# Kernel tuning notes

Measured on AMD Instinct MI355X. Metric: run time of the kernel, lower is better.

The kernel has to match this reference:

```python
import jax, jax.numpy as jnp
import numpy as np
import math

B, L, D, H = 8, 1000, 1024, 16
HD = D // H

def setup_inputs() -> dict:
    key = jax.random.key(0)
    k1, k2, k3 = jax.random.split(key, 3)
    s_in = 1.0 / math.sqrt(D)
    x = jax.random.normal(k1, (B, L, D), dtype=jnp.float32)
    Wqkv = jax.random.normal(k2, (D, 3 * D), dtype=jnp.float32) * s_in
    bqkv = jnp.zeros((3 * D,), dtype=jnp.float32)
    Wo = jax.random.normal(k3, (D, D), dtype=jnp.float32) * s_in
    bo = jnp.zeros((D,), dtype=jnp.float32)
    return {"x": x, "Wqkv": Wqkv, "bqkv": bqkv, "Wo": Wo, "bo": bo}

def reference(x, Wqkv, bqkv, Wo, bo):
    b, l, d = x.shape
    qkv = x @ Wqkv + bqkv                      # [B,L,3D]
    q, k, v = jnp.split(qkv, 3, axis=-1)       # each [B,L,D]
    q = q.reshape(b, l, H, HD)
    k = k.reshape(b, l, H, HD)
    v = v.reshape(b, l, H, HD)
    scale = 1.0 / math.sqrt(HD)
    att = jnp.einsum('blhd,bmhd->bhlm', q, k) * scale   # [B,H,L,L]
    causal = jnp.tril(jnp.ones((l, l), dtype=bool))      # [L,L]
    att = jnp.where(causal[None, None, :, :], att, -jnp.inf)
    att = jax.nn.softmax(att, axis=-1)
    out = jnp.einsum('bhlm,bmhd->blhd', att, v).reshape(b, l, d)
    return out @ Wo + bo
```

## Files before the change

### kernel.cpp

```cpp
#include <hip/hip_runtime.h>
#include <hip/hip_bf16.h>

typedef unsigned short u16;
typedef unsigned int u32;
typedef __attribute__((ext_vector_type(8))) __bf16 bf16x8;
typedef __attribute__((ext_vector_type(4))) float f32x4;
typedef __attribute__((ext_vector_type(4))) u32 u32x4;
typedef __attribute__((ext_vector_type(4))) u16 u16x4;

#define LQ 1000
#define MM 8000

__device__ __forceinline__ u16 f2bf(float f){
  __bf16 h = (__bf16)f;
  return __builtin_bit_cast(u16, h);
}
__device__ __forceinline__ void async_copy16(const void* g, void* l){
  __builtin_amdgcn_global_load_lds((const __attribute__((address_space(1))) u32*)g,
                                   (__attribute__((address_space(3))) u32*)l, 16, 0, 0);
}

__global__ __launch_bounds__(256)
void kcvt(const float* __restrict__ src, u16* __restrict__ dst, long n){
  const long i = ((long)blockIdx.x * 256 + threadIdx.x) * 4;
  if (i + 3 >= n) {
    for (long j = i; j < n; j++) dst[j] = f2bf(src[j]);
    return;
  }
  const float4 v = *(const float4*)&src[i];
  u16x4 o; o.x = f2bf(v.x); o.y = f2bf(v.y); o.z = f2bf(v.z); o.w = f2bf(v.w);
  *(u16x4*)&dst[i] = o;
}

__global__ __launch_bounds__(256)
void ktranspose_cvt(const float* __restrict__ src, u16* __restrict__ dst, int R, int C){
  __shared__ u16 tile[32][33];
  const int tx = threadIdx.x & 31, ty = threadIdx.x >> 5;
  const long bx = (long)blockIdx.x * 32, by = (long)blockIdx.y * 32;
  #pragma unroll
  for (int i = 0; i < 32; i += 8) tile[ty + i][tx] = f2bf(src[(by + ty + i) * C + bx + tx]);
  __syncthreads();
  #pragma unroll
  for (int i = 0; i < 32; i += 8) dst[(bx + ty + i) * R + by + tx] = tile[tx][ty + i];
}

template<int EPI>
__global__ __launch_bounds__(256)
void gemm128(const u16* __restrict__ A, const u16* __restrict__ BT, const float* __restrict__ bias,
             u16* __restrict__ O0, u16* __restrict__ O1, u16* __restrict__ O2,
             float* __restrict__ OF)
{
  constexpr int K = 1024;
  __shared__ __align__(16) u16 As[2][128 * 32];
  __shared__ __align__(16) u16 Bs[2][128 * 32];
  const int t = threadIdx.x, lane = t & 63, wave = t >> 6;
  const int quad = lane >> 4, l15 = lane & 15;
  const int m0 = blockIdx.y * 128, n0 = blockIdx.x * 128;
  const int wm = (wave >> 1) * 64, wn = (wave & 1) * 64;

  f32x4 acc[4][4] = {};

  const int srow = t >> 2, scol = (t & 3) * 8;
  const long aoff0 = (long)min(m0 + srow,      MM - 1) * K + scol;
  const long aoff1 = (long)min(m0 + srow + 64, MM - 1) * K + scol;
  const long boff0 = (long)(n0 + srow)      * K + scol;
  const long boff1 = (long)(n0 + srow + 64) * K + scol;
  char* AsB0 = (char*)As[0] + wave * 1024;
  char* AsB1 = (char*)As[1] + wave * 1024;
  char* BsB0 = (char*)Bs[0] + wave * 1024;
  char* BsB1 = (char*)Bs[1] + wave * 1024;

  for (int kt = 0; kt < K; kt += 64) {
    __syncthreads();
    async_copy16(A  + aoff0 + kt,      AsB0);
    async_copy16(A  + aoff1 + kt,      AsB0 + 4096);
    async_copy16(BT + boff0 + kt,      BsB0);
    async_copy16(BT + boff1 + kt,      BsB0 + 4096);
    async_copy16(A  + aoff0 + kt + 32, AsB1);
    async_copy16(A  + aoff1 + kt + 32, AsB1 + 4096);
    async_copy16(BT + boff0 + kt + 32, BsB1);
    async_copy16(BT + boff1 + kt + 32, BsB1 + 4096);
    __syncthreads();
    #pragma unroll
    for (int half = 0; half < 2; half++) {
      bf16x8 af[4], bfv[4];
      #pragma unroll
      for (int i = 0; i < 4; i++) af[i]  = *(const bf16x8*)&As[half][(wm + i * 16 + l15) * 32 + quad * 8];
      #pragma unroll
      for (int i = 0; i < 4; i++) bfv[i] = *(const bf16x8*)&Bs[half][(wn + i * 16 + l15) * 32 + quad * 8];
      #pragma unroll
      for (int mi = 0; mi < 4; mi++)
        #pragma unroll
        for (int ni = 0; ni < 4; ni++)
          acc[mi][ni] = __builtin_amdgcn_mfma_f32_16x16x32_bf16(af[mi], bfv[ni], acc[mi][ni], 0, 0, 0);
    }
  }

  float bs[4]; int cols[4];
  #pragma unroll
  for (int ni = 0; ni < 4; ni++) { cols[ni] = n0 + wn + ni * 16 + l15; bs[ni] = bias[cols[ni]]; }

  #pragma unroll
  for (int mi = 0; mi < 4; mi++) {
    #pragma unroll
    for (int r = 0; r < 4; r++) {
      const int row = m0 + wm + mi * 16 + quad * 4 + r;
      if (row >= MM) continue;
      if (EPI == 0) {
        const int b = row / 1000, l = row - b * 1000;
        #pragma unroll
        for (int ni = 0; ni < 4; ni++) {
          const u16 o = f2bf(acc[mi][ni][r] + bs[ni]);
          const int col = cols[ni];
          const int which = col >> 10, hh = (col >> 6) & 15, dd = col & 63;
          const int bh = b * 16 + hh;
          if      (which == 0) O0[((long)bh * LQ + l) * 64 + dd] = o;
          else if (which == 1) O1[((long)bh * LQ + l) * 64 + dd] = o;
          else                 O2[((long)bh * 64 + dd) * LQ + l] = o;
        }
      } else {
        #pragma unroll
        for (int ni = 0; ni < 4; ni++)
          OF[(long)row * 1024 + cols[ni]] = acc[mi][ni][r] + bs[ni];
      }
    }
  }
}

__global__ __launch_bounds__(256)
void attn_kernel(const u16* __restrict__ Qb, const u16* __restrict__ Kb,
                 const u16* __restrict__ VTb, u16* __restrict__ AO)
{
  __shared__ __align__(16) u16 Ps[4][2][16 * 40];
  const int t = threadIdx.x, lane = t & 63, wave = t >> 6;
  const int quad = lane >> 4, l15 = lane & 15;
  const int bh = blockIdx.y;
  const int c = blockIdx.x * 4 + wave;
  const u16* Q  = Qb  + (long)bh * LQ * 64;
  const u16* Kp = Kb  + (long)bh * LQ * 64;
  const u16* VT = VTb + (long)bh * 64 * LQ;
  const int b = bh >> 4, h = bh & 15;
  const float sscale = 0.18033688011112042f;

  for (int pass = 0; pass < 2; ++pass) {
    const int chunk = pass ? (31 - c) : c;
    const int qbase = chunk * 32;
    const int nkt = chunk + 1;

    int qv[2]; bf16x8 bq0[2], bq1[2];
    #pragma unroll
    for (int g = 0; g < 2; g++) {
      qv[g] = qbase + g * 16 + l15;
      const int qc = min(qv[g], LQ - 1);
      bq0[g] = *(const bf16x8*)&Q[(long)qc * 64 +      quad * 8];
      bq1[g] = *(const bf16x8*)&Q[(long)qc * 64 + 32 + quad * 8];
    }

    float l_p[2] = { 0.f, 0.f };
    f32x4 o[2][4] = {};

    bf16x8 pa00, pa01, pa10, pa11, pav0, pav1, pav2, pav3;
    {
      const int krA = min(l15, LQ - 1), krB = min(16 + l15, LQ - 1);
      pa00 = *(const bf16x8*)&Kp[(long)krA * 64 +      quad * 8];
      pa01 = *(const bf16x8*)&Kp[(long)krA * 64 + 32 + quad * 8];
      pa10 = *(const bf16x8*)&Kp[(long)krB * 64 +      quad * 8];
      pa11 = *(const bf16x8*)&Kp[(long)krB * 64 + 32 + quad * 8];
      const int vcol = min(quad * 8, LQ - 8);
      pav0 = *(const bf16x8*)&VT[(long)( 0 + l15) * LQ + vcol];
      pav1 = *(const bf16x8*)&VT[(long)(16 + l15) * LQ + vcol];
      pav2 = *(const bf16x8*)&VT[(long)(32 + l15) * LQ + vcol];
      pav3 = *(const bf16x8*)&VT[(long)(48 + l15) * LQ + vcol];
    }

    for (int kk = 0; kk < nkt; ++kk) {
      const int k0 = kk * 32;
      const bool lastt = (kk + 1 == nkt);
      const bf16x8 a00 = pa00, a01 = pa01, a10 = pa10, a11 = pa11;
      bf16x8 av[4] = { pav0, pav1, pav2, pav3 };
      if (!lastt) {
        const int n0k = k0 + 32;
        const int krA = min(n0k + l15, LQ - 1), krB = min(n0k + 16 + l15, LQ - 1);
        pa00 = *(const bf16x8*)&Kp[(long)krA * 64 +      quad * 8];
        pa01 = *(const bf16x8*)&Kp[(long)krA * 64 + 32 + quad * 8];
        pa10 = *(const bf16x8*)&Kp[(long)krB * 64 +      quad * 8];
        pa11 = *(const bf16x8*)&Kp[(long)krB * 64 + 32 + quad * 8];
        const int vcol = min(n0k + quad * 8, LQ - 8);
        pav0 = *(const bf16x8*)&VT[(long)( 0 + l15) * LQ + vcol];
        pav1 = *(const bf16x8*)&VT[(long)(16 + l15) * LQ + vcol];
        pav2 = *(const bf16x8*)&VT[(long)(32 + l15) * LQ + vcol];
        pav3 = *(const bf16x8*)&VT[(long)(48 + l15) * LQ + vcol];
      }

      #pragma unroll
      for (int g = 0; g < 2; g++) {
        const f32x4 z = {};
        f32x4 s0 = __builtin_amdgcn_mfma_f32_16x16x32_bf16(a00, bq0[g], z, 0, 0, 0);
        s0       = __builtin_amdgcn_mfma_f32_16x16x32_bf16(a01, bq1[g], s0, 0, 0, 0);
        f32x4 s1 = __builtin_amdgcn_mfma_f32_16x16x32_bf16(a10, bq0[g], z, 0, 0, 0);
        s1       = __builtin_amdgcn_mfma_f32_16x16x32_bf16(a11, bq1[g], s1, 0, 0, 0);

        float p0[4], p1[4];
        if (lastt) {
          const int q = qv[g];
          #pragma unroll
          for (int r = 0; r < 4; r++) {
            const int key0 = k0 + quad * 4 + r;
            p0[r] = __builtin_amdgcn_exp2f((key0      <= q) ? s0[r] * sscale : -3.0e38f);
            p1[r] = __builtin_amdgcn_exp2f((key0 + 16 <= q) ? s1[r] * sscale : -3.0e38f);
          }
        } else {
          #pragma unroll
          for (int r = 0; r < 4; r++) {
            p0[r] = __builtin_amdgcn_exp2f(s0[r] * sscale);
            p1[r] = __builtin_amdgcn_exp2f(s1[r] * sscale);
          }
        }
        u16x4 w0, w1; float ls = 0.f;
        #pragma unroll
        for (int r = 0; r < 4; r++) {
          w0[r] = f2bf(p0[r]); w1[r] = f2bf(p1[r]);
          ls += p0[r] + p1[r];
        }
        l_p[g] += ls;
        *(u16x4*)&Ps[wave][g][l15 * 40 + quad * 4]      = w0;
        *(u16x4*)&Ps[wave][g][l15 * 40 + 16 + quad * 4] = w1;
        const bf16x8 bp = *(const bf16x8*)&Ps[wave][g][l15 * 40 + quad * 8];
        #pragma unroll
        for (int cc = 0; cc < 4; cc++)
          o[g][cc] = __builtin_amdgcn_mfma_f32_16x16x32_bf16(av[cc], bp, o[g][cc], 0, 0, 0);
      }
    }

    #pragma unroll
    for (int g = 0; g < 2; g++) {
      if (qv[g] >= LQ) continue;
      float l = l_p[g];
      l += __shfl_xor(l, 16);
      l += __shfl_xor(l, 32);
      const float inv = 1.0f / l;
      const long base = ((long)(b * LQ + qv[g])) * 1024 + h * 64;
      #pragma unroll
      for (int cc = 0; cc < 4; cc++) {
        u16x4 w;
        #pragma unroll
        for (int r = 0; r < 4; r++) w[r] = f2bf(o[g][cc][r] * inv);
        *(u16x4*)&AO[base + cc * 16 + quad * 4] = w;
      }
    }
  }
}

extern "C" void kernel_launch(void* const* d_in, const int* in_sizes, int n_in,
                              void* d_out, int out_size, void* d_ws, size_t ws_size,
                              hipStream_t stream) {
  const float* x    = (const float*)d_in[0];
  const float* Wqkv = (const float*)d_in[1];
  const float* bqkv = (const float*)d_in[2];
  const float* Wo   = (const float*)d_in[3];
  const float* bo   = (const float*)d_in[4];
  float* out = (float*)d_out;

  char* ws = (char*)d_ws;
  u16* WqkvT = (u16*)(ws);
  u16* WoT   = (u16*)(ws + 6291456);
  u16* xb    = (u16*)(ws + 8388608);
  u16* Qb    = (u16*)(ws + 8388608 + 16384000L);
  u16* Kb    = (u16*)(ws + 8388608 + 2 * 16384000L);
  u16* VTb   = (u16*)(ws + 8388608 + 3 * 16384000L);
  u16* AO    = xb;

  kcvt<<<8000, 256, 0, stream>>>(x, xb, 8192000L);
  ktranspose_cvt<<<dim3(96, 32), 256, 0, stream>>>(Wqkv, WqkvT, 1024, 3072);
  ktranspose_cvt<<<dim3(32, 32), 256, 0, stream>>>(Wo,   WoT,   1024, 1024);
  gemm128<0><<<dim3(24, 63), 256, 0, stream>>>(xb, WqkvT, bqkv, Qb, Kb, VTb, nullptr);
  attn_kernel<<<dim3(4, 128), 256, 0, stream>>>(Qb, Kb, VTb, AO);
  gemm128<1><<<dim3(8, 63), 256, 0, stream>>>(AO, WoT, bo, nullptr, nullptr, nullptr, out);
}
```

Before: 261.3 us.

## Replace 128x128 GEMM with 256x256 multi-stage pipelined GEMM

Rewrites both projection GEMMs as 256x256-tile, 512-thread kernels with a 4-buffer LDS ring holding three stages in flight, using explicit vmcnt waits. It also XOR-swizzles LDS to avoid bank conflicts, raises MFMA priority with setprio, and remaps block IDs for L2 locality. The goal is to hide global-load latency and increase reuse per tile. In exchange it needs 128KB of dynamic LDS and more registers, and the wider tiles leave fewer blocks for the output projection grid (128 blocks).

```diff
diff --git a/kernel.cpp b/kernel.cpp
--- a/kernel.cpp
+++ b/kernel.cpp
@@ -5,7 +5,6 @@
 typedef unsigned int u32;
 typedef __attribute__((ext_vector_type(8))) __bf16 bf16x8;
 typedef __attribute__((ext_vector_type(4))) float f32x4;
-typedef __attribute__((ext_vector_type(4))) u32 u32x4;
 typedef __attribute__((ext_vector_type(4))) u16 u16x4;
 
 #define LQ 1000
@@ -45,73 +44,112 @@
 }
 
 template<int EPI>
-__global__ __launch_bounds__(256)
-void gemm128(const u16* __restrict__ A, const u16* __restrict__ BT, const float* __restrict__ bias,
+__global__ __launch_bounds__(512, 2)
+void gemm256(const u16* __restrict__ A, const u16* __restrict__ BT, const float* __restrict__ bias,
              u16* __restrict__ O0, u16* __restrict__ O1, u16* __restrict__ O2,
              float* __restrict__ OF)
 {
   constexpr int K = 1024;
-  __shared__ __align__(16) u16 As[2][128 * 32];
-  __shared__ __align__(16) u16 Bs[2][128 * 32];
+  constexpr int NT = K / 32;
+  extern __shared__ __align__(16) char lds[];
   const int t = threadIdx.x, lane = t & 63, wave = t >> 6;
   const int quad = lane >> 4, l15 = lane & 15;
-  const int m0 = blockIdx.y * 128, n0 = blockIdx.x * 128;
-  const int wm = (wave >> 1) * 64, wn = (wave & 1) * 64;
-
-  f32x4 acc[4][4] = {};
-
-  const int srow = t >> 2, scol = (t & 3) * 8;
-  const long aoff0 = (long)min(m0 + srow,      MM - 1) * K + scol;
-  const long aoff1 = (long)min(m0 + srow + 64, MM - 1) * K + scol;
-  const long boff0 = (long)(n0 + srow)      * K + scol;
-  const long boff1 = (long)(n0 + srow + 64) * K + scol;
-  char* AsB0 = (char*)As[0] + wave * 1024;
-  char* AsB1 = (char*)As[1] + wave * 1024;
-  char* BsB0 = (char*)Bs[0] + wave * 1024;
-  char* BsB1 = (char*)Bs[1] + wave * 1024;
-
-  for (int kt = 0; kt < K; kt += 64) {
-    __syncthreads();
-    async_copy16(A  + aoff0 + kt,      AsB0);
-    async_copy16(A  + aoff1 + kt,      AsB0 + 4096);
-    async_copy16(BT + boff0 + kt,      BsB0);
-    async_copy16(BT + boff1 + kt,      BsB0 + 4096);
-    async_copy16(A  + aoff0 + kt + 32, AsB1);
-    async_copy16(A  + aoff1 + kt + 32, AsB1 + 4096);
-    async_copy16(BT + boff0 + kt + 32, BsB1);
-    async_copy16(BT + boff1 + kt + 32, BsB1 + 4096);
-    __syncthreads();
-    #pragma unroll
-    for (int half = 0; half < 2; half++) {
-      bf16x8 af[4], bfv[4];
+
+  const int nwgx = gridDim.x;
+  const int nwg = nwgx * gridDim.y;
+  int bid = blockIdx.y * nwgx + blockIdx.x;
+  bid = (bid & 7) * (nwg >> 3) + (bid >> 3);
+  const int m0 = (bid / nwgx) * 256, n0 = (bid % nwgx) * 256;
+
+  const int wm = (wave >> 2) * 128, wn = (wave & 3) * 64;
+
+  const int srow  = wave * 16 + (lane >> 2);
+  const int scolg = (lane & 3) ^ ((srow >> 1) & 3);
+  const long aofs0 = (long)min(m0 + srow,       MM - 1) * K + scolg * 8;
+  const long aofs1 = (long)min(m0 + srow + 128, MM - 1) * K + scolg * 8;
+  const long bofs0 = (long)(n0 + srow)       * K + scolg * 8;
+  const long bofs1 = (long)(n0 + srow + 128) * K + scolg * 8;
+
+  const int swz = (l15 >> 1) & 3;
+  int aoff[8], boff[4];
+  #pragma unroll
+  for (int m = 0; m < 8; m++) aoff[m] = (wm + m * 16 + l15) * 64 + ((quad ^ swz) << 4);
+  #pragma unroll
+  for (int n = 0; n < 4; n++) boff[n] = 16384 + (wn + n * 16 + l15) * 64 + ((quad ^ swz) << 4);
+
+  f32x4 acc[8][4] = {};
+
+  auto STAGE_A = [&](int j){
+    char* d = lds + (j & 3) * 32768 + wave * 1024;
+    const long kt = (long)j * 32;
+    async_copy16(A + aofs0 + kt, d);
+    async_copy16(A + aofs1 + kt, d + 8192);
+  };
+  auto STAGE_B = [&](int j){
+    char* d = lds + (j & 3) * 32768 + 16384 + wave * 1024;
+    const long kt = (long)j * 32;
+    async_copy16(BT + bofs0 + kt, d);
+    async_copy16(BT + bofs1 + kt, d + 8192);
+  };
+
+  STAGE_A(0); STAGE_B(0);
+  STAGE_A(1); STAGE_B(1);
+  STAGE_A(2); STAGE_B(2);
+
+  for (int j = 0; j < NT; ++j) {
+    if (j < NT - 2)       asm volatile("s_waitcnt vmcnt(8)" ::: "memory");
+    else if (j == NT - 2) asm volatile("s_waitcnt vmcnt(4)" ::: "memory");
+    else                  asm volatile("s_waitcnt vmcnt(0)" ::: "memory");
+    __builtin_amdgcn_s_barrier();
+
+    char* buf = lds + (j & 3) * 32768;
+    bf16x8 bfr[4], afr[4];
+    #pragma unroll
+    for (int n = 0; n < 4; n++) bfr[n] = *(const bf16x8*)(buf + boff[n]);
+    #pragma unroll
+    for (int m = 0; m < 4; m++) afr[m] = *(const bf16x8*)(buf + aoff[m]);
+    if (j < NT - 3) STAGE_A(j + 3);
+
+    __builtin_amdgcn_s_setprio(1);
+    #pragma unroll
+    for (int m = 0; m < 4; m++)
       #pragma unroll
-      for (int i = 0; i < 4; i++) af[i]  = *(const bf16x8*)&As[half][(wm + i * 16 + l15) * 32 + quad * 8];
+      for (int n = 0; n < 4; n++)
+        acc[m][n] = __builtin_amdgcn_mfma_f32_16x16x32_bf16(afr[m], bfr[n], acc[m][n], 0, 0, 0);
+    __builtin_amdgcn_s_setprio(0);
+    __builtin_amdgcn_s_barrier();
+
+    #pragma unroll
+    for (int m = 0; m < 4; m++) afr[m] = *(const bf16x8*)(buf + aoff[m + 4]);
+    if (j < NT - 3) STAGE_B(j + 3);
+
+    __builtin_amdgcn_s_setprio(1);
+    #pragma unroll
+    for (int m = 0; m < 4; m++)
       #pragma unroll
-      for (int i = 0; i < 4; i++) bfv[i] = *(const bf16x8*)&Bs[half][(wn + i * 16 + l15) * 32 + quad * 8];
-      #pragma unroll
-      for (int mi = 0; mi < 4; mi++)
-        #pragma unroll
-        for (int ni = 0; ni < 4; ni++)
-          acc[mi][ni] = __builtin_amdgcn_mfma_f32_16x16x32_bf16(af[mi], bfv[ni], acc[mi][ni], 0, 0, 0);
-    }
+      for (int n = 0; n < 4; n++)
+        acc[m + 4][n] = __builtin_amdgcn_mfma_f32_16x16x32_bf16(afr[m], bfr[n], acc[m + 4][n], 0, 0, 0);
+    __builtin_amdgcn_s_setprio(0);
+
+    asm volatile("s_waitcnt lgkmcnt(0)" ::: "memory");
   }
 
   float bs[4]; int cols[4];
   #pragma unroll
-  for (int ni = 0; ni < 4; ni++) { cols[ni] = n0 + wn + ni * 16 + l15; bs[ni] = bias[cols[ni]]; }
-
-  #pragma unroll
-  for (int mi = 0; mi < 4; mi++) {
+  for (int n = 0; n < 4; n++) { cols[n] = n0 + wn + n * 16 + l15; bs[n] = bias[cols[n]]; }
+
+  #pragma unroll
+  for (int m = 0; m < 8; m++) {
     #pragma unroll
     for (int r = 0; r < 4; r++) {
-      const int row = m0 + wm + mi * 16 + quad * 4 + r;
+      const int row = m0 + wm + m * 16 + quad * 4 + r;
       if (row >= MM) continue;
       if (EPI == 0) {
         const int b = row / 1000, l = row - b * 1000;
         #pragma unroll
-        for (int ni = 0; ni < 4; ni++) {
-          const u16 o = f2bf(acc[mi][ni][r] + bs[ni]);
-          const int col = cols[ni];
+        for (int n = 0; n < 4; n++) {
+          const u16 o = f2bf(acc[m][n][r] + bs[n]);
+          const int col = cols[n];
           const int which = col >> 10, hh = (col >> 6) & 15, dd = col & 63;
           const int bh = b * 16 + hh;
           if      (which == 0) O0[((long)bh * LQ + l) * 64 + dd] = o;
@@ -120,8 +158,8 @@
         }
       } else {
         #pragma unroll
-        for (int ni = 0; ni < 4; ni++)
-          OF[(long)row * 1024 + cols[ni]] = acc[mi][ni][r] + bs[ni];
+        for (int n = 0; n < 4; n++)
+          OF[(long)row * 1024 + cols[n]] = acc[m][n][r] + bs[n];
       }
     }
   }
@@ -270,10 +308,19 @@
   u16* VTb   = (u16*)(ws + 8388608 + 3 * 16384000L);
   u16* AO    = xb;
 
+  static bool inited = false;
+  if (!inited) {
+    (void)hipFuncSetAttribute(reinterpret_cast<const void*>(&gemm256<0>),
+                              hipFuncAttributeMaxDynamicSharedMemorySize, 131072);
+    (void)hipFuncSetAttribute(reinterpret_cast<const void*>(&gemm256<1>),
+                              hipFuncAttributeMaxDynamicSharedMemorySize, 131072);
+    inited = true;
+  }
+
   kcvt<<<8000, 256, 0, stream>>>(x, xb, 8192000L);
   ktranspose_cvt<<<dim3(96, 32), 256, 0, stream>>>(Wqkv, WqkvT, 1024, 3072);
   ktranspose_cvt<<<dim3(32, 32), 256, 0, stream>>>(Wo,   WoT,   1024, 1024);
-  gemm128<0><<<dim3(24, 63), 256, 0, stream>>>(xb, WqkvT, bqkv, Qb, Kb, VTb, nullptr);
+  gemm256<0><<<dim3(12, 32), 512, 131072, stream>>>(xb, WqkvT, bqkv, Qb, Kb, VTb, nullptr);
   attn_kernel<<<dim3(4, 128), 256, 0, stream>>>(Qb, Kb, VTb, AO);
-  gemm128<1><<<dim3(8, 63), 256, 0, stream>>>(AO, WoT, bo, nullptr, nullptr, nullptr, out);
-}
+  gemm256<1><<<dim3(4, 32), 512, 131072, stream>>>(AO, WoT, bo, nullptr, nullptr, nullptr, out);
+}
```

New measurement: 276.0 us. +5.6%, slower.

## Swizzle GEMM LDS tiles and split attention query halves across waves

Applied to the files above, without the earlier changes.

The GEMM now XOR-swizzles the 16-byte column groups of each LDS row on both the async-load and fragment-read sides, to cut LDS bank conflicts on the MFMA operand reads. The attention kernel gives each wave one 16-query group instead of two and doubles the grid. This raises wave count and occupancy, at the cost of each wave loading the K/V tiles separately, which doubles global/L2 K/V traffic. s_setprio hints are also placed around the MFMA sequences so waves in the matrix phase get priority over others.

```diff
diff --git a/kernel.cpp b/kernel.cpp
--- a/kernel.cpp
+++ b/kernel.cpp
@@ -5,7 +5,6 @@
 typedef unsigned int u32;
 typedef __attribute__((ext_vector_type(8))) __bf16 bf16x8;
 typedef __attribute__((ext_vector_type(4))) float f32x4;
-typedef __attribute__((ext_vector_type(4))) u32 u32x4;
 typedef __attribute__((ext_vector_type(4))) u16 u16x4;
 
 #define LQ 1000
@@ -60,7 +59,9 @@
 
   f32x4 acc[4][4] = {};
 
-  const int srow = t >> 2, scol = (t & 3) * 8;
+  const int srow = t >> 2;
+  const int sg   = (t & 3) ^ ((srow >> 1) & 3);
+  const int scol = sg * 8;
   const long aoff0 = (long)min(m0 + srow,      MM - 1) * K + scol;
   const long aoff1 = (long)min(m0 + srow + 64, MM - 1) * K + scol;
   const long boff0 = (long)(n0 + srow)      * K + scol;
@@ -69,6 +70,8 @@
   char* AsB1 = (char*)As[1] + wave * 1024;
   char* BsB0 = (char*)Bs[0] + wave * 1024;
   char* BsB1 = (char*)Bs[1] + wave * 1024;
+
+  const int swz = (l15 >> 1) & 3;
 
   for (int kt = 0; kt < K; kt += 64) {
     __syncthreads();
@@ -85,9 +88,9 @@
     for (int half = 0; half < 2; half++) {
       bf16x8 af[4], bfv[4];
       #pragma unroll
-      for (int i = 0; i < 4; i++) af[i]  = *(const bf16x8*)&As[half][(wm + i * 16 + l15) * 32 + quad * 8];
-      #pragma unroll
-      for (int i = 0; i < 4; i++) bfv[i] = *(const bf16x8*)&Bs[half][(wn + i * 16 + l15) * 32 + quad * 8];
+      for (int i = 0; i < 4; i++) af[i]  = *(const bf16x8*)&As[half][(wm + i * 16 + l15) * 32 + (quad ^ swz) * 8];
+      #pragma unroll
+      for (int i = 0; i < 4; i++) bfv[i] = *(const bf16x8*)&Bs[half][(wn + i * 16 + l15) * 32 + (quad ^ swz) * 8];
       #pragma unroll
       for (int mi = 0; mi < 4; mi++)
         #pragma unroll
@@ -131,11 +134,12 @@
 void attn_kernel(const u16* __restrict__ Qb, const u16* __restrict__ Kb,
                  const u16* __restrict__ VTb, u16* __restrict__ AO)
 {
-  __shared__ __align__(16) u16 Ps[4][2][16 * 40];
+  __shared__ __align__(16) u16 Ps[4][16 * 40];
   const int t = threadIdx.x, lane = t & 63, wave = t >> 6;
   const int quad = lane >> 4, l15 = lane & 15;
   const int bh = blockIdx.y;
-  const int c = blockIdx.x * 4 + wave;
+  const int W = blockIdx.x * 4 + wave;
+  const int cpair = W >> 1, g = W & 1;
   const u16* Q  = Qb  + (long)bh * LQ * 64;
   const u16* Kp = Kb  + (long)bh * LQ * 64;
   const u16* VT = VTb + (long)bh * 64 * LQ;
@@ -143,21 +147,17 @@
   const float sscale = 0.18033688011112042f;
 
   for (int pass = 0; pass < 2; ++pass) {
-    const int chunk = pass ? (31 - c) : c;
+    const int chunk = pass ? (31 - cpair) : cpair;
     const int qbase = chunk * 32;
     const int nkt = chunk + 1;
 
-    int qv[2]; bf16x8 bq0[2], bq1[2];
-    #pragma unroll
-    for (int g = 0; g < 2; g++) {
-      qv[g] = qbase + g * 16 + l15;
-      const int qc = min(qv[g], LQ - 1);
-      bq0[g] = *(const bf16x8*)&Q[(long)qc * 64 +      quad * 8];
-      bq1[g] = *(const bf16x8*)&Q[(long)qc * 64 + 32 + quad * 8];
-    }
-
-    float l_p[2] = { 0.f, 0.f };
-    f32x4 o[2][4] = {};
+    const int qv = qbase + g * 16 + l15;
+    const int qc = min(qv, LQ - 1);
+    const bf16x8 bq0 = *(const bf16x8*)&Q[(long)qc * 64 +      quad * 8];
+    const bf16x8 bq1 = *(const bf16x8*)&Q[(long)qc * 64 + 32 + quad * 8];
+
+    float l_p = 0.f;
+    f32x4 o[4] = {};
 
     bf16x8 pa00, pa01, pa10, pa11, pav0, pav1, pav2, pav3;
     {
@@ -192,59 +192,57 @@
         pav3 = *(const bf16x8*)&VT[(long)(48 + l15) * LQ + vcol];
       }
 
-      #pragma unroll
-      for (int g = 0; g < 2; g++) {
-        const f32x4 z = {};
-        f32x4 s0 = __builtin_amdgcn_mfma_f32_16x16x32_bf16(a00, bq0[g], z, 0, 0, 0);
-        s0       = __builtin_amdgcn_mfma_f32_16x16x32_bf16(a01, bq1[g], s0, 0, 0, 0);
-        f32x4 s1 = __builtin_amdgcn_mfma_f32_16x16x32_bf16(a10, bq0[g], z, 0, 0, 0);
-        s1       = __builtin_amdgcn_mfma_f32_16x16x32_bf16(a11, bq1[g], s1, 0, 0, 0);
-
-        float p0[4], p1[4];
-        if (lastt) {
-          const int q = qv[g];
-          #pragma unroll
-          for (int r = 0; r < 4; r++) {
-            const int key0 = k0 + quad * 4 + r;
-            p0[r] = __builtin_amdgcn_exp2f((key0      <= q) ? s0[r] * sscale : -3.0e38f);
-            p1[r] = __builtin_amdgcn_exp2f((key0 + 16 <= q) ? s1[r] * sscale : -3.0e38f);
-          }
-        } else {
-          #pragma unroll
-          for (int r = 0; r < 4; r++) {
-            p0[r] = __builtin_amdgcn_exp2f(s0[r] * sscale);
-            p1[r] = __builtin_amdgcn_exp2f(s1[r] * sscale);
-          }
+      const f32x4 z = {};
+      __builtin_amdgcn_s_setprio(1);
+      f32x4 s0 = __builtin_amdgcn_mfma_f32_16x16x32_bf16(a00, bq0, z, 0, 0, 0);
+      s0       = __builtin_amdgcn_mfma_f32_16x16x32_bf16(a01, bq1, s0, 0, 0, 0);
+      f32x4 s1 = __builtin_amdgcn_mfma_f32_16x16x32_bf16(a10, bq0, z, 0, 0, 0);
+      s1       = __builtin_amdgcn_mfma_f32_16x16x32_bf16(a11, bq1, s1, 0, 0, 0);
+      __builtin_amdgcn_s_setprio(0);
+
+      float p0[4], p1[4];
+      if (lastt) {
+        #pragma unroll
+        for (int r = 0; r < 4; r++) {
+          const int key0 = k0 + quad * 4 + r;
+          p0[r] = __builtin_amdgcn_exp2f((key0      <= qv) ? s0[r] * sscale : -3.0e38f);
+          p1[r] = __builtin_amdgcn_exp2f((key0 + 16 <= qv) ? s1[r] * sscale : -3.0e38f);
         }
-        u16x4 w0, w1; float ls = 0.f;
+      } else {
         #pragma unroll
         for (int r = 0; r < 4; r++) {
-          w0[r] = f2bf(p0[r]); w1[r] = f2bf(p1[r]);
-          ls += p0[r] + p1[r];
+          p0[r] = __builtin_amdgcn_exp2f(s0[r] * sscale);
+          p1[r] = __builtin_amdgcn_exp2f(s1[r] * sscale);
         }
-        l_p[g] += ls;
-        *(u16x4*)&Ps[wave][g][l15 * 40 + quad * 4]      = w0;
-        *(u16x4*)&Ps[wave][g][l15 * 40 + 16 + quad * 4] = w1;
-        const bf16x8 bp = *(const bf16x8*)&Ps[wave][g][l15 * 40 + quad * 8];
-        #pragma unroll
-        for (int cc = 0; cc < 4; cc++)
-          o[g][cc] = __builtin_amdgcn_mfma_f32_16x16x32_bf16(av[cc], bp, o[g][cc], 0, 0, 0);
-      }
-    }
-
-    #pragma unroll
-    for (int g = 0; g < 2; g++) {
-      if (qv[g] >= LQ) continue;
-      float l = l_p[g];
+      }
+      u16x4 w0, w1; float ls = 0.f;
+      #pragma unroll
+      for (int r = 0; r < 4; r++) {
+        w0[r] = f2bf(p0[r]); w1[r] = f2bf(p1[r]);
+        ls += p0[r] + p1[r];
+      }
+      l_p += ls;
+      *(u16x4*)&Ps[wave][l15 * 40 + quad * 4]      = w0;
+      *(u16x4*)&Ps[wave][l15 * 40 + 16 + quad * 4] = w1;
+      const bf16x8 bp = *(const bf16x8*)&Ps[wave][l15 * 40 + quad * 8];
+      __builtin_amdgcn_s_setprio(1);
+      #pragma unroll
+      for (int cc = 0; cc < 4; cc++)
+        o[cc] = __builtin_amdgcn_mfma_f32_16x16x32_bf16(av[cc], bp, o[cc], 0, 0, 0);
+      __builtin_amdgcn_s_setprio(0);
+    }
+
+    if (qv < LQ) {
+      float l = l_p;
       l += __shfl_xor(l, 16);
       l += __shfl_xor(l, 32);
       const float inv = 1.0f / l;
-      const long base = ((long)(b * LQ + qv[g])) * 1024 + h * 64;
+      const long base = ((long)(b * LQ + qv)) * 1024 + h * 64;
       #pragma unroll
       for (int cc = 0; cc < 4; cc++) {
         u16x4 w;
         #pragma unroll
-        for (int r = 0; r < 4; r++) w[r] = f2bf(o[g][cc][r] * inv);
+        for (int r = 0; r < 4; r++) w[r] = f2bf(o[cc][r] * inv);
         *(u16x4*)&AO[base + cc * 16 + quad * 4] = w;
       }
     }
@@ -274,6 +272,6 @@
   ktranspose_cvt<<<dim3(96, 32), 256, 0, stream>>>(Wqkv, WqkvT, 1024, 3072);
   ktranspose_cvt<<<dim3(32, 32), 256, 0, stream>>>(Wo,   WoT,   1024, 1024);
   gemm128<0><<<dim3(24, 63), 256, 0, stream>>>(xb, WqkvT, bqkv, Qb, Kb, VTb, nullptr);
-  attn_kernel<<<dim3(4, 128), 256, 0, stream>>>(Qb, Kb, VTb, AO);
+  attn_kernel<<<dim3(8, 128), 256, 0, stream>>>(Qb, Kb, VTb, AO);
   gemm128<1><<<dim3(8, 63), 256, 0, stream>>>(AO, WoT, bo, nullptr, nullptr, nullptr, out);
 }
```

Result: slower. 295.6 us (+13.2%).
